# Kernel optimization log

Hardware: AMD Instinct MI355X
Metric: run time of the kernel (lower is better)

The kernel has to match this reference:

```python
import jax, jax.numpy as jnp
import numpy as np

B, N, L, Q = 10, 10, 256, 100
V, E, H = 365553, 200, 128


def _lstm_dir(x, Wi, Wh, b, rev):
    # x: [B,T,D] -> hidden states [B,T,H]; torch gate order i,f,g,o
    xg = jnp.einsum('btd,dk->btk', x, Wi) + b
    xg = jnp.swapaxes(xg, 0, 1)  # [T,B,4H]
    Bb = x.shape[0]
    Hh = Wh.shape[0]

    def step(carry, xt):
        h, c = carry
        g = xt + h @ Wh
        i, f, gg, o = jnp.split(g, 4, axis=-1)
        c = jax.nn.sigmoid(f) * c + jax.nn.sigmoid(i) * jnp.tanh(gg)
        h = jax.nn.sigmoid(o) * jnp.tanh(c)
        return (h, c), h

    init = (jnp.zeros((Bb, Hh), x.dtype), jnp.zeros((Bb, Hh), x.dtype))
    _, hs = jax.lax.scan(step, init, xg, reverse=rev)
    return jnp.swapaxes(hs, 0, 1)


def lstm_bi(x, Wi, Wh, b):
    return jnp.concatenate([_lstm_dir(x, Wi[0], Wh[0], b[0], False),
                            _lstm_dir(x, Wi[1], Wh[1], b[1], True)], axis=-1)


def setup_inputs():
    key = jax.random.key(0)
    ks = jax.random.split(key, 20)
    p = lambda k, s: jax.random.normal(k, s, jnp.float32) * 0.05
    return {
        'contents': jax.random.randint(ks[0], (B, N, L), 0, V),
        'question_ans': jax.random.randint(ks[1], (B, Q), 0, V),
        'logics': jnp.ones((B, 1), jnp.float32),
        'emb_fixed': p(ks[2], (V, E)),
        'emb_delta': p(ks[3], (V, E)),
        'ctx_Wi': p(ks[4], (2, E, 4 * H)), 'ctx_Wh': p(ks[5], (2, H, 4 * H)), 'ctx_b': p(ks[6], (2, 4 * H)),
        'qr_Wi': p(ks[7], (2, 2 * H + 2, 4 * H)), 'qr_Wh': p(ks[8], (2, H, 4 * H)), 'qr_b': p(ks[9], (2, 4 * H)),
        'cr_Wi': p(ks[10], (2, 4 * H + 2, 4 * H)), 'cr_Wh': p(ks[11], (2, H, 4 * H)), 'cr_b': p(ks[12], (2, 4 * H)),
        'gate_r_W': p(ks[13], (2 * H, 1)), 'gate_r_b': p(ks[14], (1,)),
        'gate_n_W': p(ks[15], (4 * H, 1)), 'gate_n_b': p(ks[16], (1,)),
        'dec_W': p(ks[17], (8 * H, 1)), 'dec_b': p(ks[18], (1,)),
    }


def _forward(contents, question_ans, logics, emb_fixed, emb_delta,
             ctx_Wi, ctx_Wh, ctx_b, qr_Wi, qr_Wh, qr_b, cr_Wi, cr_Wh, cr_b,
             gate_r_W, gate_r_b, gate_n_W, gate_n_b, dec_W, dec_b):
    # embeddings: fixed + trainable delta
    q_vec = emb_fixed[question_ans] + emb_delta[question_ans]            # [B,Q,200]
    q_enc = lstm_bi(q_vec, ctx_Wi, ctx_Wh, ctx_b)                        # [B,Q,256]
    c_tok = contents.reshape(B * N, L)
    c_vec = emb_fixed[c_tok] + emb_delta[c_tok]
    D_enc = lstm_bi(c_vec, ctx_Wi, ctx_Wh, ctx_b).reshape(B, N, L, 2 * H)  # [B,N,L,256]

    # reasoning gates (FC + sigmoid), +1e-8 as in source
    gate_q = jax.nn.sigmoid(q_enc @ gate_r_W + gate_r_b) + 1e-8          # [B,Q,1]
    gate_c = jax.nn.sigmoid(D_enc @ gate_r_W + gate_r_b) + 1e-8          # [B,N,L,1]

    # question-content matching matrix, all docs at once
    M_qc = jnp.einsum('bqd,bnld->bnql', q_enc, D_enc)                    # [B,N,Q,L]
    an = jax.nn.softmax(M_qc, axis=3)
    bn = jax.nn.softmax(M_qc, axis=2)
    RnQ = jnp.einsum('bnql,bnld->bnqd', an, D_enc)                       # [B,N,Q,256]
    RnD = jnp.einsum('bnql,bqd->bnld', bn, q_enc)                        # [B,N,L,256]
    D_RnD = jnp.concatenate([D_enc, RnD], axis=-1)                       # [B,N,L,512]
    feat_row = jnp.stack([M_qc.max(axis=2), M_qc.mean(axis=2)], axis=-1)  # [B,N,L,2]
    feat_col = jnp.stack([M_qc.max(axis=3), M_qc.mean(axis=3)], axis=-1)  # [B,N,Q,2]

    # cross-document attention: scores over all (position m, doc j) jointly per row
    Mx = jnp.einsum('bild,bjmd->bilmj', D_RnD, D_RnD)                    # [B,N,L,L,N]
    beta = jax.nn.softmax(Mx.reshape(B, N, L, L * N), axis=-1).reshape(B, N, L, L, N)
    RmD = jnp.einsum('bilmj,bjmd->bild', beta, D_RnD)                    # [B,N,L,512]

    RnQ_in = jnp.concatenate([RnQ, feat_col], axis=-1) * gate_q[:, None]  # [B,N,Q,258]
    RmD_in = jnp.concatenate([RmD, feat_row], axis=-1) * gate_c           # [B,N,L,514]

    q_out = lstm_bi(RnQ_in.reshape(B * N, Q, 2 * H + 2), qr_Wi, qr_Wh, qr_b).max(axis=1)
    c_out = lstm_bi(RmD_in.reshape(B * N, L, 4 * H + 2), cr_Wi, cr_Wh, cr_b).max(axis=1)
    feat = jnp.concatenate([q_out, c_out], axis=-1).reshape(B, N, 4 * H)  # [B,N,512]

    g = jax.nn.sigmoid(feat @ gate_n_W + gate_n_b)                        # [B,N,1]
    gf = feat * g
    dec_in = jnp.concatenate([gf.max(axis=1), gf.mean(axis=1)], axis=-1)  # [B,1024]
    dec = dec_in @ dec_W + dec_b                                          # [B,1]
    return (dec * logics).reshape(B // 5, 5)


def reference(contents, question_ans, logics, emb_fixed, emb_delta,
              ctx_Wi, ctx_Wh, ctx_b, qr_Wi, qr_Wh, qr_b, cr_Wi, cr_Wh, cr_b,
              gate_r_W, gate_r_b, gate_n_W, gate_n_b, dec_W, dec_b):
    return _forward(contents, question_ans, logics, emb_fixed, emb_delta,
                    ctx_Wi, ctx_Wh, ctx_b, qr_Wi, qr_Wh, qr_b, cr_Wi, cr_Wh, cr_b,
                    gate_r_W, gate_r_b, gate_n_W, gate_n_b, dec_W, dec_b)
```

## Files before the change

kernel.cpp:

```cpp
#include <hip/hip_runtime.h>
#include <cstdint>
#include <cstddef>

typedef __attribute__((ext_vector_type(8))) _Float16 half8;
typedef __attribute__((ext_vector_type(4))) float f32x4;

__device__ __forceinline__ float fexp(float x){ return __expf(x); }
__device__ __forceinline__ float sig_fast(float x){
  return __builtin_amdgcn_rcpf(1.f + __expf(-x));
}
__device__ __forceinline__ float tanh_fast(float x){
  return 2.f*__builtin_amdgcn_rcpf(1.f + __expf(-2.f*x)) - 1.f;
}
__device__ __forceinline__ float sigf(float x){ return 1.0f/(1.0f+expf(-x)); }

__device__ __forceinline__ void async_lds16(const _Float16* g, _Float16* l){
  __builtin_amdgcn_global_load_lds(
      (const __attribute__((address_space(1))) void*)g,
      (__attribute__((address_space(3))) void*)l, 16, 0, 0);
}

__global__ __launch_bounds__(64)
void k_sentinel(float* out, int n){ int i=threadIdx.x; if(i<n) out[i]=1.0e9f; }

__global__ __launch_bounds__(256)
void k_embed16u(const int* __restrict__ c_tok, const int* __restrict__ q_tok,
                const float* __restrict__ ef, const float* __restrict__ ed,
                _Float16* __restrict__ oh, _Float16* __restrict__ ol, int Kpad)
{
  int t = blockIdx.x; int e = threadIdx.x;
  if (e >= Kpad) return;
  _Float16 h = (_Float16)0.f, l = (_Float16)0.f;
  int tok = -1;
  if (t < 25600) tok = c_tok[t];
  else if (t < 26600) tok = q_tok[t - 25600];
  if (tok >= 0 && e < 200){
    long r = (long)tok*200 + e;
    float v = ef[r] + ed[r];
    h = (_Float16)v; l = (_Float16)(v - (float)h);
  }
  oh[(long)t*Kpad + e] = h;
  ol[(long)t*Kpad + e] = l;
}

__global__ __launch_bounds__(256)
void k_wsplit(const float* __restrict__ W, _Float16* __restrict__ th,
              _Float16* __restrict__ tl, int K, int Kpad)
{
  int n = blockIdx.x;
  int dir = n >> 9, col = n & 511;
  for (int k = threadIdx.x; k < Kpad; k += 256){
    _Float16 h = (_Float16)0.f, l = (_Float16)0.f;
    if (k < K){
      float v = W[((long)dir*K + k)*512 + col];
      h = (_Float16)v; l = (_Float16)(v - (float)h);
    }
    th[(long)n*Kpad + k] = h;
    tl[(long)n*Kpad + k] = l;
  }
}

#define MFMA16(a,b,c) __builtin_amdgcn_mfma_f32_16x16x32_f16(a,b,c,0,0,0)

__global__ __launch_bounds__(256, 2)
void k_mfma(const _Float16* __restrict__ Ahb, const _Float16* __restrict__ Alb,
            const _Float16* __restrict__ Bhb, const _Float16* __restrict__ Blb,
            float* __restrict__ Cb, int M, int K, int N, int ldc,
            long sA, long sB, long sC, int divA, int divB)
{
  const int z = blockIdx.z;
  const _Float16* Ah = Ahb + (long)(z/divA)*sA;
  const _Float16* Al = Alb + (long)(z/divA)*sA;
  const _Float16* Bh = Bhb + (long)(z/divB)*sB;
  const _Float16* Bl = Blb + (long)(z/divB)*sB;
  float* C = Cb + (long)z*sC;

  const int m0 = blockIdx.x*128, n0 = blockIdx.y*128;
  const int tid = threadIdx.x;
  const int lane = tid & 63, wave = tid >> 6;
  const int wm = wave >> 1, wn = wave & 1;

  __shared__ _Float16 lds[2][2048*8];

  f32x4 acc[4][4] = {};

  const int KT = K >> 5;

  auto STAGE = [&](int buf, int kt){
    const int k0 = kt*32;
    #pragma unroll
    for (int it = 0; it < 8; ++it){
      const int c  = it*256 + tid;
      const int op = it >> 1;
      const int kb = (c >> 7) & 3;
      const int row = c & 127;
      const _Float16* base = (op==0) ? Ah : (op==1) ? Al : (op==2) ? Bh : Bl;
      int gr = (op < 2) ? (m0 + row) : (n0 + row);
      if (op < 2 && gr >= M) gr = M - 1;
      const _Float16* src = base + (long)gr*K + k0 + kb*8;
      _Float16* dst = &lds[buf][(size_t)(it*256 + (tid & ~63))*8];
      async_lds16(src, dst);
    }
  };

  auto COMPUTE = [&](int buf){
    const int kb = lane >> 4, r = lane & 15;
    half8 ah[4], al[4], bh[4], bl[4];
    #pragma unroll
    for (int mi = 0; mi < 4; ++mi){
      ah[mi] = *(const half8*)&lds[buf][(size_t)(        kb*128 + wm*64 + mi*16 + r)*8];
      al[mi] = *(const half8*)&lds[buf][(size_t)( 512 + kb*128 + wm*64 + mi*16 + r)*8];
    }
    #pragma unroll
    for (int ni = 0; ni < 4; ++ni){
      bh[ni] = *(const half8*)&lds[buf][(size_t)(1024 + kb*128 + wn*64 + ni*16 + r)*8];
      bl[ni] = *(const half8*)&lds[buf][(size_t)(1536 + kb*128 + wn*64 + ni*16 + r)*8];
    }
    #pragma unroll
    for (int mi = 0; mi < 4; ++mi)
      #pragma unroll
      for (int ni = 0; ni < 4; ++ni){
        acc[mi][ni] = MFMA16(ah[mi], bh[ni], acc[mi][ni]);
        acc[mi][ni] = MFMA16(ah[mi], bl[ni], acc[mi][ni]);
        acc[mi][ni] = MFMA16(al[mi], bh[ni], acc[mi][ni]);
      }
  };

  STAGE(0, 0);
  for (int kt = 0; kt < KT; ++kt){
    __syncthreads();
    if (kt + 1 < KT) STAGE((kt+1)&1, kt+1);
    COMPUTE(kt&1);
  }

  const int r4 = (lane >> 4) * 4, cN = lane & 15;
  #pragma unroll
  for (int mi = 0; mi < 4; ++mi)
    #pragma unroll
    for (int ni = 0; ni < 4; ++ni){
      const int row = m0 + wm*64 + mi*16 + r4;
      const int col = n0 + wn*64 + ni*16 + cN;
      #pragma unroll
      for (int r = 0; r < 4; ++r)
        if (row + r < M) C[(long)(row + r)*ldc + col] = acc[mi][ni][r];
    }
}

__global__ __launch_bounds__(512, 1)
void k_lstm2(const float* __restrict__ xg0, const float* __restrict__ Wh0,
             const float* __restrict__ bs0, float* __restrict__ out0,
             int S0, int T0, int ldx0,
             const float* __restrict__ xg1, const float* __restrict__ Wh1,
             const float* __restrict__ bs1, float* __restrict__ out1,
             int T1, int ldx1)
{
  const int bx = blockIdx.x;
  const int dir = blockIdx.y;
  const float* xg; const float* Whb; const float* bsb; float* out;
  int T, ldx, s;
  if (bx < S0){ s = bx;      xg = xg0; Whb = Wh0; bsb = bs0; out = out0; T = T0; ldx = ldx0; }
  else        { s = bx - S0; xg = xg1; Whb = Wh1; bsb = bs1; out = out1; T = T1; ldx = ldx1; }
  xg += dir*512;
  const float* Wh = Whb + (long)dir*128*512;
  const int dirOff = dir*128;
  const int k = threadIdx.x;
  const float bv = bsb[dir*512 + k];

  float4 wv[32];
  #pragma unroll
  for (int j = 0; j < 32; ++j){
    wv[j].x = Wh[(j*4+0)*512 + k];
    wv[j].y = Wh[(j*4+1)*512 + k];
    wv[j].z = Wh[(j*4+2)*512 + k];
    wv[j].w = Wh[(j*4+3)*512 + k];
  }

  __shared__ __align__(16) float h_lds[128];
  __shared__ float a_lds[512];
  float c = 0.f;
  if (k < 128) h_lds[k] = 0.f;
  __syncthreads();

  float gcur = xg[((long)s*T + (dir ? T-1 : 0))*ldx + k];

  for (int tt = 0; tt < T; ++tt) {
    const int t = dir ? (T-1-tt) : tt;
    float gnext = 0.f;
    if (tt + 1 < T){
      const int tn = dir ? (T-2-tt) : (tt+1);
      gnext = xg[((long)s*T + tn)*ldx + k];
    }
    float acc0 = gcur + bv, acc1 = 0.f, acc2 = 0.f, acc3 = 0.f;
    #pragma unroll
    for (int j = 0; j < 8; ++j) {
      float4 h0 = *(const float4*)&h_lds[(j*4+0)*4];
      float4 h1 = *(const float4*)&h_lds[(j*4+1)*4];
      float4 h2 = *(const float4*)&h_lds[(j*4+2)*4];
      float4 h3 = *(const float4*)&h_lds[(j*4+3)*4];
      acc0 += h0.x*wv[j*4+0].x + h0.y*wv[j*4+0].y + h0.z*wv[j*4+0].z + h0.w*wv[j*4+0].w;
      acc1 += h1.x*wv[j*4+1].x + h1.y*wv[j*4+1].y + h1.z*wv[j*4+1].z + h1.w*wv[j*4+1].w;
      acc2 += h2.x*wv[j*4+2].x + h2.y*wv[j*4+2].y + h2.z*wv[j*4+2].z + h2.w*wv[j*4+2].w;
      acc3 += h3.x*wv[j*4+3].x + h3.y*wv[j*4+3].y + h3.z*wv[j*4+3].z + h3.w*wv[j*4+3].w;
    }
    float g = (acc0 + acc1) + (acc2 + acc3);
    a_lds[k] = ((k >> 7) == 2) ? tanh_fast(g) : sig_fast(g);
    __syncthreads();
    if (k < 128) {
      float ig = a_lds[k];
      float fg = a_lds[k+128];
      float gg = a_lds[k+256];
      float og = a_lds[k+384];
      c = fg*c + ig*gg;
      float h = og*tanh_fast(c);
      h_lds[k] = h;
      out[((long)s*T + t)*256 + dirOff + k] = h;
    }
    __syncthreads();
    gcur = gnext;
  }
}

__global__ __launch_bounds__(256)
void k_gate(const float* __restrict__ in, const float* __restrict__ w,
            const float* __restrict__ b, float* __restrict__ out, int R)
{
  int row = blockIdx.x*4 + (threadIdx.x >> 6);
  int lane = threadIdx.x & 63;
  if (row >= R) return;
  const float* p = in + (long)row*256;
  float s = 0.f;
  #pragma unroll
  for (int j = 0; j < 4; ++j) s += p[lane + j*64]*w[lane + j*64];
  #pragma unroll
  for (int off = 32; off; off >>= 1) s += __shfl_down(s, off);
  if (lane == 0) out[row] = sigf(s + b[0]) + 1e-8f;
}

__global__ __launch_bounds__(256)
void k_an_feat16(const float* __restrict__ Mq, _Float16* __restrict__ anh,
                 _Float16* __restrict__ anl, float* __restrict__ feat)
{
  long r = blockIdx.x;
  int t = threadIdx.x;
  __shared__ float red[256];
  float v = Mq[r*256 + t];
  red[t] = v; __syncthreads();
  for (int s2=128;s2;s2>>=1){ if(t<s2) red[t]=fmaxf(red[t],red[t+s2]); __syncthreads(); }
  float mx = red[0]; __syncthreads();
  red[t] = v; __syncthreads();
  for (int s2=128;s2;s2>>=1){ if(t<s2) red[t]+=red[t+s2]; __syncthreads(); }
  float sv = red[0]; __syncthreads();
  float e = fexp(v - mx);
  red[t] = e; __syncthreads();
  for (int s2=128;s2;s2>>=1){ if(t<s2) red[t]+=red[t+s2]; __syncthreads(); }
  float se = red[0];
  float a = e / se;
  _Float16 h = (_Float16)a;
  anh[r*256 + t] = h;
  anl[r*256 + t] = (_Float16)(a - (float)h);
  if (t == 0){ feat[r*2] = mx; feat[r*2+1] = sv*(1.f/256.f); }
}

__global__ __launch_bounds__(256)
void k_bn_feat16(const float* __restrict__ Mq, _Float16* __restrict__ bth,
                 _Float16* __restrict__ btl, float* __restrict__ feat)
{
  int bn = blockIdx.x;
  int l = threadIdx.x;
  const float* Mb = Mq + (long)bn*25600;
  float mx = -3.4e38f, sv = 0.f;
  for (int q = 0; q < 100; ++q){ float v = Mb[q*256 + l]; mx = fmaxf(mx, v); sv += v; }
  float se = 0.f;
  for (int q = 0; q < 100; ++q) se += fexp(Mb[q*256 + l] - mx);
  float inv = 1.f/se;
  long base = ((long)bn*256 + l)*128;
  for (int q = 0; q < 100; ++q){
    float a = fexp(Mb[q*256 + l] - mx)*inv;
    _Float16 h = (_Float16)a;
    bth[base + q] = h;
    btl[base + q] = (_Float16)(a - (float)h);
  }
  for (int q = 100; q < 128; ++q){ bth[base+q] = (_Float16)0.f; btl[base+q] = (_Float16)0.f; }
  long fr = (long)(bn*256 + l)*2;
  feat[fr] = mx; feat[fr+1] = sv*0.01f;
}

__global__ __launch_bounds__(256)
void k_copy_to_x(const float* __restrict__ D, float* __restrict__ X)
{
  long idx = (long)blockIdx.x*256 + threadIdx.x;
  long r = idx >> 8; int d = idx & 255;
  X[r*512 + d] = D[idx];
}

__global__ __launch_bounds__(256)
void k_split_hl(const float* __restrict__ x, _Float16* __restrict__ h,
                _Float16* __restrict__ l, long n)
{
  long i = (long)blockIdx.x*256 + threadIdx.x;
  if (i >= n) return;
  float v = x[i];
  _Float16 hi = (_Float16)v;
  h[i] = hi;
  l[i] = (_Float16)(v - (float)hi);
}

__global__ __launch_bounds__(256)
void k_transp_hl(const float* __restrict__ src, _Float16* __restrict__ th,
                 _Float16* __restrict__ tl, int R, int Kp, long sSrc, long sDst)
{
  __shared__ float tile[32][33];
  const int m0 = blockIdx.x*32, n0 = blockIdx.y*32, z = blockIdx.z;
  const float* S = src + (long)z*sSrc;
  const int tx = threadIdx.x & 31, ty = threadIdx.x >> 5;
  #pragma unroll
  for (int r = 0; r < 32; r += 8){
    int gr = m0 + ty + r;
    tile[ty+r][tx] = (gr < R) ? S[(long)gr*256 + n0 + tx] : 0.f;
  }
  __syncthreads();
  const long base = (long)z*sDst;
  #pragma unroll
  for (int r = 0; r < 32; r += 8){
    float v = tile[tx][ty+r];
    _Float16 h = (_Float16)v;
    long o2 = base + (long)(n0+ty+r)*Kp + m0+tx;
    th[o2] = h;
    tl[o2] = (_Float16)(v - (float)h);
  }
}

__global__ __launch_bounds__(256)
void k_transpose_hl(const float* __restrict__ X, _Float16* __restrict__ Th,
                    _Float16* __restrict__ Tl)
{
  __shared__ float tile[32][33];
  const int m0 = blockIdx.x*32, n0 = blockIdx.y*32, b = blockIdx.z;
  const float* Xb = X + (long)b*2560*512;
  const int tx = threadIdx.x & 31, ty = threadIdx.x >> 5;
  #pragma unroll
  for (int r = 0; r < 32; r += 8)
    tile[ty+r][tx] = Xb[(long)(m0+ty+r)*512 + n0+tx];
  __syncthreads();
  const long base = (long)b*512*2560;
  #pragma unroll
  for (int r = 0; r < 32; r += 8){
    float v = tile[tx][ty+r];
    _Float16 h = (_Float16)v;
    long o2 = base + (long)(n0+ty+r)*2560 + m0+tx;
    Th[o2] = h;
    Tl[o2] = (_Float16)(v - (float)h);
  }
}

__global__ __launch_bounds__(256)
void k_softmax2560_hl2(const float* __restrict__ Sb, long sS,
                       _Float16* __restrict__ Shb, _Float16* __restrict__ Slb,
                       long sP)
{
  const int z = blockIdx.y;
  const float* p = Sb + z*sS + (long)blockIdx.x*2560;
  _Float16* Sh = Shb + z*sP;
  _Float16* Sl = Slb + z*sP;
  long r = blockIdx.x;
  int t = threadIdx.x;
  float loc[10];
  float mx = -3.4e38f;
  #pragma unroll
  for (int i=0;i<10;++i){ loc[i] = p[t + i*256]; mx = fmaxf(mx, loc[i]); }
  __shared__ float red[256];
  red[t]=mx; __syncthreads();
  for (int s2=128;s2;s2>>=1){ if(t<s2) red[t]=fmaxf(red[t],red[t+s2]); __syncthreads(); }
  mx = red[0]; __syncthreads();
  float se=0.f;
  #pragma unroll
  for (int i=0;i<10;++i){ loc[i]=fexp(loc[i]-mx); se+=loc[i]; }
  red[t]=se; __syncthreads();
  for (int s2=128;s2;s2>>=1){ if(t<s2) red[t]+=red[t+s2]; __syncthreads(); }
  float inv = 1.f/red[0];
  #pragma unroll
  for (int i=0;i<10;++i){
    float v = loc[i]*inv;
    _Float16 h = (_Float16)v;
    Sh[r*2560 + t + i*256] = h;
    Sl[r*2560 + t + i*256] = (_Float16)(v - (float)h);
  }
}

__global__ __launch_bounds__(320)
void k_build_rnq16(const float* __restrict__ RnQ, const float* __restrict__ featc,
                   const float* __restrict__ gq, _Float16* __restrict__ oh,
                   _Float16* __restrict__ ol)
{
  int row = blockIdx.x;
  int t = threadIdx.x;
  if (t >= 288) return;
  int b = row / 1000, q = row % 100;
  float g = gq[b*100 + q];
  float v = 0.f;
  if (t < 256)      v = RnQ[(long)row*256 + t]*g;
  else if (t < 258) v = featc[(long)row*2 + (t-256)]*g;
  _Float16 h = (_Float16)v;
  oh[(long)row*288 + t] = h;
  ol[(long)row*288 + t] = (_Float16)(v - (float)h);
}

__global__ __launch_bounds__(256)
void k_build_rmd16(const float* __restrict__ RmD, const float* __restrict__ featr,
                   const float* __restrict__ gc, _Float16* __restrict__ oh,
                   _Float16* __restrict__ ol)
{
  int row = blockIdx.x;
  float g = gc[row];
  for (int j = threadIdx.x; j < 544; j += 256){
    float v = 0.f;
    if (j < 512)      v = RmD[(long)row*512 + j]*g;
    else if (j < 514) v = featr[(long)row*2 + (j-512)]*g;
    _Float16 h = (_Float16)v;
    oh[(long)row*544 + j] = h;
    ol[(long)row*544 + j] = (_Float16)(v - (float)h);
  }
}

__global__ __launch_bounds__(256)
void k_maxt2(const float* __restrict__ hs0, float* __restrict__ o0, int S0, int T0,
             const float* __restrict__ hs1, float* __restrict__ o1, int T1)
{
  int x = blockIdx.x; int d = threadIdx.x;
  const float* hs; float* op; int T, s;
  if (x < S0){ hs = hs0; op = o0; T = T0; s = x; }
  else       { hs = hs1; op = o1; T = T1; s = x - S0; }
  float m = -3.4e38f;
  for (int t = 0; t < T; ++t) m = fmaxf(m, hs[((long)s*T + t)*256 + d]);
  op[s*256 + d] = m;
}

__global__ __launch_bounds__(512)
void k_final(const float* __restrict__ q_out, const float* __restrict__ c_out,
             const float* __restrict__ gnW, const float* __restrict__ gnB,
             const float* __restrict__ decW, const float* __restrict__ decB,
             const float* __restrict__ logics, float* __restrict__ out)
{
  int b = blockIdx.x;
  int t = threadIdx.x;
  __shared__ float red[512];
  float mx = -3.4e38f, sm = 0.f;
  for (int n = 0; n < 10; ++n) {
    int s = b*10 + n;
    float f = (t < 256) ? q_out[(long)s*256 + t] : c_out[(long)s*256 + (t-256)];
    red[t] = f * gnW[t]; __syncthreads();
    for (int st=256; st; st>>=1){ if (t<st) red[t]+=red[t+st]; __syncthreads(); }
    float g = sigf(red[0] + gnB[0]);
    __syncthreads();
    float gf = f*g;
    mx = fmaxf(mx, gf); sm += gf;
  }
  sm *= 0.1f;
  red[t] = mx*decW[t] + sm*decW[512 + t]; __syncthreads();
  for (int st=256; st; st>>=1){ if (t<st) red[t]+=red[t+st]; __syncthreads(); }
  if (t == 0) out[b] = (red[0] + decB[0]) * logics[b];
}

static inline int cdiv(int a, int b){ return (a + b - 1)/b; }

extern "C" void kernel_launch(void* const* d_in, const int* in_sizes, int n_in,
                              void* d_out, int out_size, void* d_ws, size_t ws_size,
                              hipStream_t stream)
{
  const int*   contents = (const int*)  d_in[0];
  const int*   qa       = (const int*)  d_in[1];
  const float* logics   = (const float*)d_in[2];
  const float* ef       = (const float*)d_in[3];
  const float* ed       = (const float*)d_in[4];
  const float* ctx_Wi   = (const float*)d_in[5];
  const float* ctx_Wh   = (const float*)d_in[6];
  const float* ctx_b    = (const float*)d_in[7];
  const float* qr_Wi    = (const float*)d_in[8];
  const float* qr_Wh    = (const float*)d_in[9];
  const float* qr_b     = (const float*)d_in[10];
  const float* cr_Wi    = (const float*)d_in[11];
  const float* cr_Wh    = (const float*)d_in[12];
  const float* cr_b     = (const float*)d_in[13];
  const float* grW      = (const float*)d_in[14];
  const float* grB      = (const float*)d_in[15];
  const float* gnW      = (const float*)d_in[16];
  const float* gnB      = (const float*)d_in[17];
  const float* decW     = (const float*)d_in[18];
  const float* decB     = (const float*)d_in[19];
  float* out = (float*)d_out;
  float* w = (float*)d_ws;

  const long RU = 26624;
  size_t o = 0;
  auto alloc = [&](size_t n){ size_t r = o; o += (n + 63) & ~(size_t)63; return r; };
  size_t cv16    = alloc((size_t)RU*224);
  size_t ctxW16  = alloc(1024u*224);
  size_t qrW16   = alloc(1024u*288);
  size_t crW16   = alloc(1024u*544);
  size_t c_xg    = alloc((size_t)RU*1024);
  size_t q_enc   = alloc(1000u*256);
  size_t D_enc   = alloc(25600u*256);
  size_t gate_q  = alloc(1000);
  size_t gate_c  = alloc(25600);
  size_t M_qc    = alloc(2560000);
  size_t an_     = alloc(2560000);
  size_t bn_     = alloc(3276800);
  size_t featc   = alloc(20000);
  size_t featr   = alloc(51200);
  size_t RnQ     = alloc(2560000);
  size_t Xb      = alloc(10u*2560*512);
  size_t Sbuf    = alloc(6553600);
  size_t RmD     = alloc(10u*2560*512);
  size_t rnq16   = alloc(10000u*288);
  size_t qr_xg   = alloc(10000u*1024);
  size_t q_hs    = alloc(100u*100*256);
  size_t rmd16   = alloc(25600u*544);
  size_t c_hs    = alloc(100u*256*256);
  size_t q_out   = alloc(100u*256);
  size_t c_out   = alloc(100u*256);

  if (ws_size < o*sizeof(float)) {
    k_sentinel<<<1,64,0,stream>>>(out, out_size);
    return;
  }

  _Float16* cvh = (_Float16*)(w + cv16);       _Float16* cvl = cvh + RU*224;
  _Float16* cWh = (_Float16*)(w + ctxW16);     _Float16* cWl = cWh + 1024L*224;
  _Float16* qWh = (_Float16*)(w + qrW16);      _Float16* qWl = qWh + 1024L*288;
  _Float16* rWh = (_Float16*)(w + crW16);      _Float16* rWl = rWh + 1024L*544;
  _Float16* nqh = (_Float16*)(w + rnq16);      _Float16* nql = nqh + 10000L*288;
  _Float16* mdh = (_Float16*)(w + rmd16);      _Float16* mdl = mdh + 25600L*544;
  _Float16* Xh  = (_Float16*)(w + c_xg);
  _Float16* Xl  = Xh  + 13107200L;
  _Float16* Xth = Xl  + 13107200L;
  _Float16* Xtl = Xth + 13107200L;
  _Float16* Sh  = (_Float16*)(w + M_qc);
  _Float16* Sl  = Sh + 6553600L;
  float*    S2  = w + qr_xg;
  _Float16* Sh2 = (_Float16*)(w + rmd16);
  _Float16* Sl2 = Sh2 + 6553600L;
  const long sS_pair = (long)(S2 - (w + Sbuf));
  const long sP_pair = (long)(Sh2 - Sh);
  _Float16* anh = (_Float16*)(w + an_);        _Float16* anl = anh + 2560000L;
  _Float16* bth = (_Float16*)(w + bn_);        _Float16* btl = bth + 3276800L;
  _Float16* D16h = (_Float16*)(w + RmD);       _Float16* D16l = D16h + 6553600L;
  _Float16* Dt16h = (_Float16*)(w + Sbuf);     _Float16* Dt16l = Dt16h + 6553600L;
  _Float16* q16h = (_Float16*)(w + q_hs);      _Float16* q16l = q16h + 256000L;
  _Float16* qt16h = q16l + 256000L;            _Float16* qt16l = qt16h + 327680L;
  float* q_xg_p = w + c_xg + 25600L*1024;

  k_wsplit<<<1024,256,0,stream>>>(ctx_Wi, cWh, cWl, 200, 224);
  k_wsplit<<<1024,256,0,stream>>>(qr_Wi,  qWh, qWl, 258, 288);
  k_wsplit<<<1024,256,0,stream>>>(cr_Wi,  rWh, rWl, 514, 544);
  k_embed16u<<<(int)RU, 256, 0, stream>>>(contents, qa, ef, ed, cvh, cvl, 224);

  k_mfma<<<dim3(208,8,1),256,0,stream>>>(cvh, cvl, cWh, cWl, w+c_xg,
      (int)RU, 224, 1024, 1024, 0L,0L,0L, 1,1);

  k_lstm2<<<dim3(110,2),512,0,stream>>>(
      w+c_xg, ctx_Wh, ctx_b, w+D_enc, 100, 256, 1024,
      q_xg_p, ctx_Wh, ctx_b, w+q_enc, 100, 1024);

  k_gate<<<cdiv(1000,4),256,0,stream>>>(w+q_enc, grW, grB, w+gate_q, 1000);
  k_gate<<<cdiv(25600,4),256,0,stream>>>(w+D_enc, grW, grB, w+gate_c, 25600);

  k_split_hl<<<cdiv(6553600,256),256,0,stream>>>(w+D_enc, D16h, D16l, 6553600L);
  k_split_hl<<<cdiv(256000,256),256,0,stream>>>(w+q_enc, q16h, q16l, 256000L);
  k_transp_hl<<<dim3(8,8,100),256,0,stream>>>(w+D_enc, Dt16h, Dt16l, 256, 256, 65536L, 65536L);
  k_transp_hl<<<dim3(4,8,10),256,0,stream>>>(w+q_enc, qt16h, qt16l, 100, 128, 25600L, 32768L);

  k_mfma<<<dim3(1,2,100),256,0,stream>>>(q16h, q16l, D16h, D16l, w+M_qc,
      100, 256, 256, 256, 25600L, 65536L, 25600L, 10, 1);

  k_an_feat16<<<10000,256,0,stream>>>(w+M_qc, anh, anl, w+featc);
  k_bn_feat16<<<100,256,0,stream>>>(w+M_qc, bth, btl, w+featr);

  k_mfma<<<dim3(1,2,100),256,0,stream>>>(anh, anl, Dt16h, Dt16l, w+RnQ,
      100, 256, 256, 256, 25600L, 65536L, 25600L, 1, 1);

  k_mfma<<<dim3(2,2,100),256,0,stream>>>(bth, btl, qt16h, qt16l, w+Xb+256,
      256, 128, 256, 512, 32768L, 32768L, 131072L, 1, 10);

  k_copy_to_x<<<25600,256,0,stream>>>(w+D_enc, w+Xb);

  k_split_hl<<<51200,256,0,stream>>>(w+Xb, Xh, Xl, 13107200L);
  k_transpose_hl<<<dim3(80,16,10),256,0,stream>>>(w+Xb, Xth, Xtl);

  for (int bp = 0; bp < 5; ++bp) {
    const long xo = (long)bp*2*1310720;
    k_mfma<<<dim3(20,20,2),256,0,stream>>>(Xh+xo, Xl+xo, Xh+xo, Xl+xo, w+Sbuf,
        2560, 512, 2560, 2560, 1310720L, 1310720L, sS_pair, 1, 1);
    k_softmax2560_hl2<<<dim3(2560,2),256,0,stream>>>(w+Sbuf, sS_pair, Sh, Sl, sP_pair);
    k_mfma<<<dim3(20,4,2),256,0,stream>>>(Sh, Sl, Xth+xo, Xtl+xo, w+RmD+xo,
        2560, 2560, 512, 512, sP_pair, 1310720L, 1310720L, 1, 1);
  }

  k_build_rnq16<<<10000,320,0,stream>>>(w+RnQ, w+featc, w+gate_q, nqh, nql);
  k_mfma<<<dim3(79,8,1),256,0,stream>>>(nqh, nql, qWh, qWl, w+qr_xg,
      10000, 288, 1024, 1024, 0L,0L,0L, 1,1);
  k_build_rmd16<<<25600,256,0,stream>>>(w+RmD, w+featr, w+gate_c, mdh, mdl);
  k_mfma<<<dim3(200,8,1),256,0,stream>>>(mdh, mdl, rWh, rWl, w+c_xg,
      25600, 544, 1024, 1024, 0L,0L,0L, 1,1);

  k_lstm2<<<dim3(200,2),512,0,stream>>>(
      w+c_xg, cr_Wh, cr_b, w+c_hs, 100, 256, 1024,
      w+qr_xg, qr_Wh, qr_b, w+q_hs, 100, 1024);

  k_maxt2<<<200,256,0,stream>>>(w+c_hs, w+c_out, 100, 256, w+q_hs, w+q_out, 100);

  k_final<<<10,512,0,stream>>>(w+q_out, w+c_out, gnW, gnB, decW, decB, logics, out);
}
```

Measured before the change: 2.246 ms.

## Process two LSTM sequences per block and stream recurrent weights from cache

The recurrent LSTM kernel now handles a pair of sequences per block, halving the block count. Each thread reads its column of Wh from global memory (L1/L2) on every step instead of keeping 128 weights in registers, and the two sequences share those loads. Both the context and re-encoding LSTM launches are halved. The intent is to cut register pressure and block count on the serial LSTM. The cost is per-step global weight loads, which could add latency on the critical recurrent path.

```diff
diff --git a/kernel.cpp b/kernel.cpp
--- a/kernel.cpp
+++ b/kernel.cpp
@@ -147,76 +147,79 @@
 }
 
 __global__ __launch_bounds__(512, 1)
-void k_lstm2(const float* __restrict__ xg0, const float* __restrict__ Wh0,
-             const float* __restrict__ bs0, float* __restrict__ out0,
-             int S0, int T0, int ldx0,
-             const float* __restrict__ xg1, const float* __restrict__ Wh1,
-             const float* __restrict__ bs1, float* __restrict__ out1,
-             int T1, int ldx1)
+void k_lstm2p(const float* __restrict__ xg0, const float* __restrict__ Wh0,
+              const float* __restrict__ bs0, float* __restrict__ out0,
+              int P0, int T0, int ldx0,
+              const float* __restrict__ xg1, const float* __restrict__ Wh1,
+              const float* __restrict__ bs1, float* __restrict__ out1,
+              int T1, int ldx1)
 {
   const int bx = blockIdx.x;
   const int dir = blockIdx.y;
   const float* xg; const float* Whb; const float* bsb; float* out;
-  int T, ldx, s;
-  if (bx < S0){ s = bx;      xg = xg0; Whb = Wh0; bsb = bs0; out = out0; T = T0; ldx = ldx0; }
-  else        { s = bx - S0; xg = xg1; Whb = Wh1; bsb = bs1; out = out1; T = T1; ldx = ldx1; }
+  int T, ldx, p;
+  if (bx < P0){ p = bx;      xg = xg0; Whb = Wh0; bsb = bs0; out = out0; T = T0; ldx = ldx0; }
+  else        { p = bx - P0; xg = xg1; Whb = Wh1; bsb = bs1; out = out1; T = T1; ldx = ldx1; }
   xg += dir*512;
-  const float* Wh = Whb + (long)dir*128*512;
+  const int k = threadIdx.x;
+  const float* Wh = Whb + (long)dir*128*512 + k;
   const int dirOff = dir*128;
-  const int k = threadIdx.x;
   const float bv = bsb[dir*512 + k];
 
-  float4 wv[32];
-  #pragma unroll
-  for (int j = 0; j < 32; ++j){
-    wv[j].x = Wh[(j*4+0)*512 + k];
-    wv[j].y = Wh[(j*4+1)*512 + k];
-    wv[j].z = Wh[(j*4+2)*512 + k];
-    wv[j].w = Wh[(j*4+3)*512 + k];
-  }
-
-  __shared__ __align__(16) float h_lds[128];
-  __shared__ float a_lds[512];
+  __shared__ __align__(16) float h_lds[2][128];
+  __shared__ float a_lds[2][512];
+  if (k < 128){ h_lds[0][k] = 0.f; h_lds[1][k] = 0.f; }
   float c = 0.f;
-  if (k < 128) h_lds[k] = 0.f;
   __syncthreads();
 
-  float gcur = xg[((long)s*T + (dir ? T-1 : 0))*ldx + k];
+  const long base0 = (long)(2*p)*T, base1 = base0 + T;
+  const int tfirst = dir ? T-1 : 0;
+  float g0 = xg[(base0 + tfirst)*ldx + k];
+  float g1 = xg[(base1 + tfirst)*ldx + k];
 
   for (int tt = 0; tt < T; ++tt) {
     const int t = dir ? (T-1-tt) : tt;
-    float gnext = 0.f;
+    float n0 = 0.f, n1 = 0.f;
     if (tt + 1 < T){
       const int tn = dir ? (T-2-tt) : (tt+1);
-      gnext = xg[((long)s*T + tn)*ldx + k];
-    }
-    float acc0 = gcur + bv, acc1 = 0.f, acc2 = 0.f, acc3 = 0.f;
+      n0 = xg[(base0 + tn)*ldx + k];
+      n1 = xg[(base1 + tn)*ldx + k];
+    }
+    float a00 = g0 + bv, a01 = 0.f, a02 = 0.f, a03 = 0.f;
+    float a10 = g1 + bv, a11 = 0.f, a12 = 0.f, a13 = 0.f;
     #pragma unroll
-    for (int j = 0; j < 8; ++j) {
-      float4 h0 = *(const float4*)&h_lds[(j*4+0)*4];
-      float4 h1 = *(const float4*)&h_lds[(j*4+1)*4];
-      float4 h2 = *(const float4*)&h_lds[(j*4+2)*4];
-      float4 h3 = *(const float4*)&h_lds[(j*4+3)*4];
-      acc0 += h0.x*wv[j*4+0].x + h0.y*wv[j*4+0].y + h0.z*wv[j*4+0].z + h0.w*wv[j*4+0].w;
-      acc1 += h1.x*wv[j*4+1].x + h1.y*wv[j*4+1].y + h1.z*wv[j*4+1].z + h1.w*wv[j*4+1].w;
-      acc2 += h2.x*wv[j*4+2].x + h2.y*wv[j*4+2].y + h2.z*wv[j*4+2].z + h2.w*wv[j*4+2].w;
-      acc3 += h3.x*wv[j*4+3].x + h3.y*wv[j*4+3].y + h3.z*wv[j*4+3].z + h3.w*wv[j*4+3].w;
-    }
-    float g = (acc0 + acc1) + (acc2 + acc3);
-    a_lds[k] = ((k >> 7) == 2) ? tanh_fast(g) : sig_fast(g);
+    for (int j = 0; j < 32; ++j) {
+      float4 ha = *(const float4*)&h_lds[0][j*4];
+      float4 hb = *(const float4*)&h_lds[1][j*4];
+      float w0 = Wh[(j*4+0)*512];
+      float w1 = Wh[(j*4+1)*512];
+      float w2 = Wh[(j*4+2)*512];
+      float w3 = Wh[(j*4+3)*512];
+      a00 += ha.x*w0; a10 += hb.x*w0;
+      a01 += ha.y*w1; a11 += hb.y*w1;
+      a02 += ha.z*w2; a12 += hb.z*w2;
+      a03 += ha.w*w3; a13 += hb.w*w3;
+    }
+    float G0 = (a00 + a01) + (a02 + a03);
+    float G1 = (a10 + a11) + (a12 + a13);
+    const bool istanh = ((k >> 7) == 2);
+    a_lds[0][k] = istanh ? tanh_fast(G0) : sig_fast(G0);
+    a_lds[1][k] = istanh ? tanh_fast(G1) : sig_fast(G1);
     __syncthreads();
-    if (k < 128) {
-      float ig = a_lds[k];
-      float fg = a_lds[k+128];
-      float gg = a_lds[k+256];
-      float og = a_lds[k+384];
+    if (k < 256) {
+      const int sq = k >> 7, kk = k & 127;
+      const float* av = a_lds[sq];
+      float ig = av[kk];
+      float fg = av[kk+128];
+      float gg = av[kk+256];
+      float og = av[kk+384];
       c = fg*c + ig*gg;
       float h = og*tanh_fast(c);
-      h_lds[k] = h;
-      out[((long)s*T + t)*256 + dirOff + k] = h;
+      h_lds[sq][kk] = h;
+      out[((sq ? base1 : base0) + t)*256 + dirOff + kk] = h;
     }
     __syncthreads();
-    gcur = gnext;
+    g0 = n0; g1 = n1;
   }
 }
 
@@ -557,8 +560,8 @@
   k_mfma<<<dim3(208,8,1),256,0,stream>>>(cvh, cvl, cWh, cWl, w+c_xg,
       (int)RU, 224, 1024, 1024, 0L,0L,0L, 1,1);
 
-  k_lstm2<<<dim3(110,2),512,0,stream>>>(
-      w+c_xg, ctx_Wh, ctx_b, w+D_enc, 100, 256, 1024,
+  k_lstm2p<<<dim3(55,2),512,0,stream>>>(
+      w+c_xg, ctx_Wh, ctx_b, w+D_enc, 50, 256, 1024,
       q_xg_p, ctx_Wh, ctx_b, w+q_enc, 100, 1024);
 
   k_gate<<<cdiv(1000,4),256,0,stream>>>(w+q_enc, grW, grB, w+gate_q, 1000);
@@ -602,8 +605,8 @@
   k_mfma<<<dim3(200,8,1),256,0,stream>>>(mdh, mdl, rWh, rWl, w+c_xg,
       25600, 544, 1024, 1024, 0L,0L,0L, 1,1);
 
-  k_lstm2<<<dim3(200,2),512,0,stream>>>(
-      w+c_xg, cr_Wh, cr_b, w+c_hs, 100, 256, 1024,
+  k_lstm2p<<<dim3(100,2),512,0,stream>>>(
+      w+c_xg, cr_Wh, cr_b, w+c_hs, 50, 256, 1024,
       w+qr_xg, qr_Wh, qr_b, w+q_hs, 100, 1024);
 
   k_maxt2<<<200,256,0,stream>>>(w+c_hs, w+c_out, 100, 256, w+q_hs, w+q_out, 100);
```

Result: slower. 3.015 ms (+34.2%).
